# Performance work log

Hardware: AMD Instinct MI355X
Metric: run time of the kernel (lower is better)

## Reference

```python
import jax, jax.numpy as jnp
import numpy as np

N_NODES = 100000
N_EDGES = 1000000
N_QUERY = 100000
F_IN = 64
HIDDEN = 64
LABEL_DIM = 2


def setup_inputs() -> dict:
    key = jax.random.key(0)
    ks = jax.random.split(key, 16)
    inp = {}
    for i, nm in enumerate(["Xr", "Xi", "Xj", "Xk"]):
        inp[nm] = jax.random.normal(ks[i], (N_NODES, F_IN), dtype=jnp.float32)
    for i, nm in enumerate(["norm_r", "norm_i", "norm_j", "norm_k"]):
        inp[nm] = jax.random.normal(ks[4 + i], (N_EDGES,), dtype=jnp.float32) * 0.1
    inp["edge_index"] = jax.random.randint(ks[8], (2, N_EDGES), 0, N_NODES)
    inp["query_edges"] = jax.random.randint(ks[9], (N_QUERY, 2), 0, N_NODES)
    s1 = (2.0 / (F_IN + HIDDEN)) ** 0.5  # glorot
    inp["W1"] = jax.random.normal(ks[10], (4, F_IN, HIDDEN), dtype=jnp.float32) * s1
    inp["b1"] = jnp.zeros((4, HIDDEN), dtype=jnp.float32)
    s2 = (2.0 / (HIDDEN + HIDDEN)) ** 0.5
    inp["W2"] = jax.random.normal(ks[11], (4, HIDDEN, HIDDEN), dtype=jnp.float32) * s2
    inp["b2"] = jnp.zeros((4, HIDDEN), dtype=jnp.float32)
    inp["Cw"] = jax.random.normal(ks[12], (LABEL_DIM, 8 * HIDDEN), dtype=jnp.float32) * 0.05
    inp["Cb"] = jnp.zeros((LABEL_DIM,), dtype=jnp.float32)
    return inp


def _quaconv(Xs, src, dst, norms, W, b, n_nodes):
    # Xs: list of 4 [N,F] components; norms: list of 4 [E] Laplacian norms.
    # P[a][b] = propagate(X_a, -norm_b) = scatter_add over dst of (-norm_b)_e * X_a[src_e]
    P = []
    for a in range(4):
        G = Xs[a][src]  # [E, F] gather, reused for all 4 norms
        P.append([jax.ops.segment_sum((-norms[b])[:, None] * G, dst, num_segments=n_nodes)
                  for b in range(4)])
    Tr = P[0][0] - P[1][1] - P[2][2] - P[3][3]
    Ti = P[1][0] + P[0][1] + P[3][2] - P[2][3]
    Tj = P[2][0] - P[3][1] + P[0][2] + P[1][3]
    Tk = P[3][0] + P[2][1] - P[1][2] + P[0][3]
    Wr, Wi, Wj, Wk = W[0], W[1], W[2], W[3]
    out_r = Tr @ Wr - Ti @ Wi - Tj @ Wj - Tk @ Wk + b[0]
    out_i = Tr @ Wi + Ti @ Wr + Tj @ Wk - Tk @ Wj + b[1]
    out_j = Tr @ Wj - Ti @ Wk + Tj @ Wr + Tk @ Wi + b[2]
    out_k = Tr @ Wk + Ti @ Wj - Tj @ Wi + Tk @ Wr + b[3]
    return out_r, out_i, out_j, out_k


def _forward(Xr, Xi, Xj, Xk, norm_r, norm_i, norm_j, norm_k,
             W1, b1, W2, b2, Cw, Cb, edge_index, query_edges):
    src, dst = edge_index[0], edge_index[1]
    n = Xr.shape[0]
    norms = [norm_r, norm_i, norm_j, norm_k]
    Xs = [Xr, Xi, Xj, Xk]
    for W, b in ((W1, b1), (W2, b2)):
        Xs = list(_quaconv(Xs, src, dst, norms, W, b, n))
        # complex_relu_layer_different: mask = 1.0*(x>=0); mask*x == relu(x)
        Xs = [jax.nn.relu(x) for x in Xs]
    q0, q1 = query_edges[:, 0], query_edges[:, 1]
    # cat(real[q0], real[q1], imag_i[q0], imag_i[q1], ...) -> [Eq, 8*hidden]
    feats = jnp.concatenate([c[idx] for c in Xs for idx in (q0, q1)], axis=-1)
    # dropout is identity at inference; Conv1d(kernel=1) == linear over channels
    logits = feats @ Cw.T + Cb  # [Eq, label_dim]
    return jax.nn.log_softmax(logits, axis=-1)


def reference(Xr, Xi, Xj, Xk, norm_r, norm_i, norm_j, norm_k,
              W1, b1, W2, b2, Cw, Cb, edge_index, query_edges):
    return _forward(Xr, Xi, Xj, Xk, norm_r, norm_i, norm_j, norm_k,
                    W1, b1, W2, b2, Cw, Cb, edge_index, query_edges)
```

## Files before the change

kernel.cpp:

```cpp
#include <hip/hip_runtime.h>
#include <hip/hip_bf16.h>

#define N_NODESC 100000
#define N_EDGESC 1000000
#define N_QUERYC 100000
#define CNT_STRIDE 8

typedef short short8 __attribute__((ext_vector_type(8)));
typedef short s16x2 __attribute__((ext_vector_type(2)));
typedef float f32x4 __attribute__((ext_vector_type(4)));

__device__ __forceinline__ float ldf(const void* p, int i, int isbf) {
  return isbf ? __bfloat162float(((const __hip_bfloat16*)p)[i])
              : ((const float*)p)[i];
}
__device__ __forceinline__ unsigned short f2b(float x) {
  __hip_bfloat16 h = __float2bfloat16(x);
  return *(unsigned short*)&h;
}
__device__ __forceinline__ float b2f(unsigned int u) {
  return __uint_as_float(u << 16);
}
__device__ __forceinline__ s16x2 u2s(unsigned u) {
  union { unsigned u; s16x2 s; } c; c.u = u; return c.s;
}
__device__ __forceinline__ void gload16(const void* g, void* l) {
  __builtin_amdgcn_global_load_lds(
      (const __attribute__((address_space(1))) void*)g,
      (__attribute__((address_space(3))) void*)l, 16, 0, 0);
}

__global__ void k_prep(const void* x, int* flag, int* cnt, int nc) {
  int bid = blockIdx.x;
  int t = threadIdx.x;
  if (bid == 0) {
    __shared__ int scnt;
    if (t == 0) scnt = 0;
    __syncthreads();
    const unsigned short* h = (const unsigned short*)x;
    int local = 0;
    for (int i = t; i < 4096; i += 256) {
      int e = (h[i] >> 7) & 0xFF;
      if (e >= 107 && e <= 133) local++;
    }
    atomicAdd(&scnt, local);
    __syncthreads();
    if (t == 0) *flag = (scnt >= 3482) ? 1 : 0;
  } else {
    int i = (bid - 1) * 256 + t;
    if (i < nc) cnt[i] = 0;
  }
}

__global__ __launch_bounds__(256) void k_fill0_ilv(
    const int* __restrict__ ei,
    const void* nr, const void* ni, const void* nj, const void* nk,
    int* __restrict__ cnt, uint4* __restrict__ temp, int ne, int fillBlocks,
    const void* X0, const void* X1, const void* X2, const void* X3,
    const int* __restrict__ flagp, unsigned short* __restrict__ Xg, int n) {
  int bid = blockIdx.x;
  if (bid < fillBlocks) {
    int isbf = *flagp;
    int e = bid * 256 + threadIdx.x;
    if (e >= ne) return;
    int s = ei[e];
    int d = ei[ne + e];
    int pos = atomicAdd(&cnt[d * CNT_STRIDE], 1);
    uint4 r;
    r.x = (unsigned)s;
    r.y = (unsigned)f2b(-ldf(nr, e, isbf)) | ((unsigned)f2b(-ldf(ni, e, isbf)) << 16);
    r.z = (unsigned)f2b(-ldf(nj, e, isbf)) | ((unsigned)f2b(-ldf(nk, e, isbf)) << 16);
    r.w = (unsigned)pos;
    temp[e] = r;
  } else {
    int isbf = *flagp;
    int lane = threadIdx.x & 63;
    int node = (bid - fillBlocks) * 4 + (threadIdx.x >> 6);
    if (node >= n) return;
    int idx = node * 64 + lane;
    unsigned int lo = f2b(ldf(X0, idx, isbf)) | ((unsigned int)f2b(ldf(X1, idx, isbf)) << 16);
    unsigned int hi = f2b(ldf(X2, idx, isbf)) | ((unsigned int)f2b(ldf(X3, idx, isbf)) << 16);
    uint2 g = make_uint2(lo, hi);
    *(uint2*)(Xg + (size_t)node * 256 + lane * 4) = g;
  }
}

__global__ void k_scan1(const int* __restrict__ cnt, int* __restrict__ off,
                        int* __restrict__ partials, int n) {
  __shared__ int s[1024];
  int t = threadIdx.x;
  int idx = blockIdx.x * 1024 + t;
  int v = (idx < n) ? cnt[idx * CNT_STRIDE] : 0;
  s[t] = v;
  __syncthreads();
  for (int d = 1; d < 1024; d <<= 1) {
    int tmp = (t >= d) ? s[t - d] : 0;
    __syncthreads();
    s[t] += tmp;
    __syncthreads();
  }
  if (idx < n) off[idx] = s[t] - v;
  if (t == 1023) partials[blockIdx.x] = s[1023];
}

__global__ void k_scan2(const int* __restrict__ partials, int* __restrict__ pref,
                        int* __restrict__ off, int nb, int npos) {
  __shared__ int s[128];
  int t = threadIdx.x;
  int v = (t < nb) ? partials[t] : 0;
  s[t] = v;
  __syncthreads();
  for (int d = 1; d < 128; d <<= 1) {
    int tmp = (t >= d) ? s[t - d] : 0;
    __syncthreads();
    s[t] += tmp;
    __syncthreads();
  }
  if (t < nb) pref[t] = s[t] - v;
  if (t == 127) off[npos] = s[127];
}

__global__ void k_scan3(int* __restrict__ off, const int* __restrict__ pref, int n) {
  int i = blockIdx.x * 256 + threadIdx.x;
  if (i < n) off[i] = off[i] + pref[i >> 10];
}

__global__ void k_scatter(const int* __restrict__ ei, const uint4* __restrict__ temp,
                          const int* __restrict__ off, uint4* __restrict__ recs, int ne) {
  int e = blockIdx.x * 256 + threadIdx.x;
  if (e >= ne) return;
  uint4 r = temp[e];
  int d = ei[ne + e];
  int pos = (int)r.w;
  recs[off[d] + pos] = r;
}

#if __has_builtin(__builtin_amdgcn_fdot2_f32_bf16)
#define USE_DOT2 1
#else
#define USE_DOT2 0
#endif
__global__ __launch_bounds__(128, 8) void k_agg(
    const unsigned short* __restrict__ Xg, const int* __restrict__ off,
    const uint4* __restrict__ recs, unsigned short* __restrict__ Tf, int nnodes) {
  __shared__ unsigned short tl4[2][4][256];
  int lane = threadIdx.x & 63;
  int w = threadIdx.x >> 6;
  int gq = blockIdx.x * 2 + w;
  int n0 = gq * 4;
  if (n0 >= nnodes) return;

  int o_[5];
#pragma unroll
  for (int i = 0; i < 5; i++) o_[i] = __builtin_amdgcn_readfirstlane(off[n0 + i]);

#pragma unroll
  for (int n = 0; n < 4; ++n) {
    int rs = o_[n], re = o_[n + 1];
    float tr = 0.f, ti = 0.f, tj = 0.f, tk = 0.f;

    auto qacc = [&](uint2 g, unsigned mx, unsigned my) {
#if USE_DOT2
      unsigned a = mx, b = my;
      unsigned sa = (a >> 16) | (a << 16);
      unsigned sb = (b >> 16) | (b << 16);
      unsigned A1 = a ^ 0x80000000u;
      unsigned A2 = b ^ 0x80008000u;
      unsigned B2 = sb ^ 0x00008000u;
      unsigned D2 = sb ^ 0x80000000u;
      s16x2 gx = u2s(g.x), gy = u2s(g.y);
      tr = __builtin_amdgcn_fdot2_f32_bf16(u2s(A1), gx, tr, false);
      tr = __builtin_amdgcn_fdot2_f32_bf16(u2s(A2), gy, tr, false);
      ti = __builtin_amdgcn_fdot2_f32_bf16(u2s(sa), gx, ti, false);
      ti = __builtin_amdgcn_fdot2_f32_bf16(u2s(B2), gy, ti, false);
      tj = __builtin_amdgcn_fdot2_f32_bf16(u2s(b),  gx, tj, false);
      tj = __builtin_amdgcn_fdot2_f32_bf16(u2s(A1), gy, tj, false);
      tk = __builtin_amdgcn_fdot2_f32_bf16(u2s(D2), gx, tk, false);
      tk = __builtin_amdgcn_fdot2_f32_bf16(u2s(sa), gy, tk, false);
#else
      float mr = __uint_as_float(mx << 16), mi = __uint_as_float(mx & 0xffff0000u);
      float mj = __uint_as_float(my << 16), mk = __uint_as_float(my & 0xffff0000u);
      float xr = __uint_as_float(g.x << 16), xi = __uint_as_float(g.x & 0xffff0000u);
      float xj = __uint_as_float(g.y << 16), xk = __uint_as_float(g.y & 0xffff0000u);
      tr += mr * xr - mi * xi - mj * xj - mk * xk;
      ti += mr * xi + mi * xr + mj * xk - mk * xj;
      tj += mr * xj - mi * xk + mj * xr + mk * xi;
      tk += mr * xk + mi * xj - mj * xi + mk * xr;
#endif
    };

    int e = rs;
    for (; e + 8 <= re; e += 8) {
      uint4 r[8];
#pragma unroll
      for (int u = 0; u < 8; u++) r[u] = recs[e + u];
      int ss[8];
      unsigned sx[8], sy[8];
#pragma unroll
      for (int u = 0; u < 8; u++) {
        ss[u] = __builtin_amdgcn_readfirstlane((int)r[u].x);
        sx[u] = __builtin_amdgcn_readfirstlane(r[u].y);
        sy[u] = __builtin_amdgcn_readfirstlane(r[u].z);
      }
      uint2 g[8];
#pragma unroll
      for (int u = 0; u < 8; u++)
        g[u] = *(const uint2*)(Xg + (size_t)ss[u] * 256 + lane * 4);
#pragma unroll
      for (int u = 0; u < 8; u++) qacc(g[u], sx[u], sy[u]);
    }
    for (; e < re; ++e) {
      uint4 r = recs[e];
      int s = __builtin_amdgcn_readfirstlane((int)r.x);
      unsigned mx = __builtin_amdgcn_readfirstlane(r.y);
      unsigned my = __builtin_amdgcn_readfirstlane(r.z);
      uint2 g0 = *(const uint2*)(Xg + (size_t)s * 256 + lane * 4);
      qacc(g0, mx, my);
    }

    tl4[w][n][lane] = f2b(tr);
    tl4[w][n][64 + lane] = f2b(ti);
    tl4[w][n][128 + lane] = f2b(tj);
    tl4[w][n][192 + lane] = f2b(tk);
  }
  __builtin_amdgcn_wave_barrier();

  size_t blk = (size_t)(gq >> 2) * 4096;
  int qi = gq & 3;
#pragma unroll
  for (int h = 0; h < 2; ++h) {
    int m = h * 64 + lane;
    int n = m & 3, l = m >> 2;
    uint4 v = *(const uint4*)&tl4[w][n][l * 8];
    size_t o = blk + (size_t)(l >> 2) * 512 + (l & 3) * 128 + qi * 32 + n * 8;
    *(uint4*)(Tf + o) = v;
  }
}

__global__ void k_weff2(const void* W1, const void* b1, const void* W2, const void* b2,
                        const int* __restrict__ flagp,
                        unsigned short* __restrict__ Wq1, float* __restrict__ bcat1,
                        unsigned short* __restrict__ Wq2, float* __restrict__ bcat2) {
  int isbf = *flagp;
  int layer = blockIdx.x >> 6;
  const void* W = layer ? W2 : W1;
  const void* b = layer ? b2 : b1;
  unsigned short* Wq = layer ? Wq2 : Wq1;
  float* bcat = layer ? bcat2 : bcat1;
  int t = (blockIdx.x & 63) * 256 + threadIdx.x;
  int w4 = t >> 12;
  int h = (t >> 6) & 63;
  int kk = t & 63;
  int s = (kk >> 3) ^ (h & 7);
  Wq[(w4 * 64 + h) * 64 + s * 8 + (kk & 7)] = f2b(ldf(W, w4 * 4096 + kk * 64 + h, isbf));
  if (t < 256) bcat[t] = ldf(b, t, isbf);
}

__global__ __launch_bounds__(256, 2) void k_gemm(
    const unsigned short* __restrict__ A, const unsigned short* __restrict__ Wq,
    const float* __restrict__ bias, int M, int mode,
    unsigned short* __restrict__ XgOut,
    float* __restrict__ P, const void* Cw, const int* __restrict__ flagp) {
  __shared__ unsigned short Wsm[16384];

  int t = threadIdx.x;
  int lane = t & 63;
  int w = t >> 6;
  int l15 = lane & 15, quad = lane >> 4;
  int m0 = blockIdx.x * 64;
  int hh = (w & 1) * 32;

#pragma unroll
  for (int i = 0; i < 8; i++)
    gload16((const char*)Wq + (size_t)(i * 256 + t) * 16,
            (char*)Wsm + (size_t)(i * 256 + w * 64) * 16);
  __syncthreads();

  short8 av[2][8];
  int n16 = blockIdx.x * 4 + (w >> 1) * 2;
#pragma unroll
  for (int mi = 0; mi < 2; mi++)
#pragma unroll
    for (int kc = 0; kc < 8; kc++)
      av[mi][kc] = *(const short8*)(A + (size_t)(n16 + mi) * 4096 + kc * 512 + lane * 8);

  f32x4 acc[2][4][2];
#pragma unroll
  for (int mi = 0; mi < 2; mi++)
#pragma unroll
    for (int c = 0; c < 4; c++)
#pragma unroll
      for (int hb = 0; hb < 2; hb++) acc[mi][c][hb] = (f32x4){0.f, 0.f, 0.f, 0.f};

#pragma unroll
  for (int kc = 0; kc < 8; kc++) {
    int a = kc >> 1;
    short8 bv[4][2];
#pragma unroll
    for (int c = 0; c < 4; c++) {
      int w4 = a ^ c;
      int neg = (0x3950 >> (a * 4 + c)) & 1;
#pragma unroll
      for (int hb = 0; hb < 2; hb++) {
        int h = hh + hb * 16 + l15;
        int lc = ((kc & 1) * 4 + quad) ^ (l15 & 7);
        short8 bb = *(const short8*)&Wsm[(w4 * 64 + h) * 64 + lc * 8];
        if (neg) {
          uint4 u = *(uint4*)&bb;
          u.x ^= 0x80008000u; u.y ^= 0x80008000u;
          u.z ^= 0x80008000u; u.w ^= 0x80008000u;
          bb = *(short8*)&u;
        }
        bv[c][hb] = bb;
      }
    }
#pragma unroll
    for (int mi = 0; mi < 2; mi++)
#pragma unroll
      for (int c = 0; c < 4; c++)
#pragma unroll
        for (int hb = 0; hb < 2; hb++)
          acc[mi][c][hb] =
              __builtin_amdgcn_mfma_f32_16x16x32_bf16(av[mi][kc], bv[c][hb], acc[mi][c][hb], 0, 0, 0);
  }

  float bias_v[4][2];
#pragma unroll
  for (int c = 0; c < 4; c++)
#pragma unroll
    for (int hb = 0; hb < 2; hb++) bias_v[c][hb] = bias[c * 64 + hh + hb * 16 + l15];

  if (mode == 0) {
#pragma unroll
    for (int mi = 0; mi < 2; mi++) {
#pragma unroll
      for (int hb = 0; hb < 2; hb++) {
#pragma unroll
        for (int r = 0; r < 4; r++) {
          int node = m0 + (w >> 1) * 32 + mi * 16 + quad * 4 + r;
          unsigned int lo =
              f2b(fmaxf(acc[mi][0][hb][r] + bias_v[0][hb], 0.f)) |
              ((unsigned int)f2b(fmaxf(acc[mi][1][hb][r] + bias_v[1][hb], 0.f)) << 16);
          unsigned int hi =
              f2b(fmaxf(acc[mi][2][hb][r] + bias_v[2][hb], 0.f)) |
              ((unsigned int)f2b(fmaxf(acc[mi][3][hb][r] + bias_v[3][hb], 0.f)) << 16);
          *(uint2*)(XgOut + (size_t)node * 256 + (hh + hb * 16 + l15) * 4) =
              make_uint2(lo, hi);
        }
      }
    }
  } else {
    int isbf = *flagp;
    float cw[4][2][4];
#pragma unroll
    for (int c = 0; c < 4; c++)
#pragma unroll
      for (int hb = 0; hb < 2; hb++) {
        int h = hh + hb * 16 + l15;
#pragma unroll
        for (int d = 0; d < 2; d++)
#pragma unroll
          for (int e = 0; e < 2; e++)
            cw[c][hb][e + 2 * d] = ldf(Cw, d * 512 + c * 128 + e * 64 + h, isbf);
      }
    float* Pout = P + ((hh == 0) ? 0 : 4);
#pragma unroll
    for (int mi = 0; mi < 2; mi++) {
#pragma unroll
      for (int r = 0; r < 4; r++) {
        int node = m0 + (w >> 1) * 32 + mi * 16 + quad * 4 + r;
        float pd0 = 0.f, pd1 = 0.f, pd2 = 0.f, pd3 = 0.f;
#pragma unroll
        for (int c = 0; c < 4; c++)
#pragma unroll
          for (int hb = 0; hb < 2; hb++) {
            float v = fmaxf(acc[mi][c][hb][r] + bias_v[c][hb], 0.f);
            pd0 += v * cw[c][hb][0];
            pd1 += v * cw[c][hb][1];
            pd2 += v * cw[c][hb][2];
            pd3 += v * cw[c][hb][3];
          }
#pragma unroll
        for (int o = 1; o < 16; o <<= 1) {
          pd0 += __shfl_xor(pd0, o);
          pd1 += __shfl_xor(pd1, o);
          pd2 += __shfl_xor(pd2, o);
          pd3 += __shfl_xor(pd3, o);
        }
        if (l15 == 0 && node < M) {
          f32x4 st = {pd0, pd1, pd2, pd3};
          *(f32x4*)(Pout + (size_t)node * 8) = st;
        }
      }
    }
  }
}

__global__ void k_query(const int* __restrict__ qe, const float* __restrict__ P,
                        const void* Cb, const int* __restrict__ flagp,
                        void* out, int nq) {
  int isbf = *flagp;
  int q = blockIdx.x * 256 + threadIdx.x;
  if (q >= nq) return;
  int q0 = qe[q * 2], q1 = qe[q * 2 + 1];
  f32x4 a0 = *(const f32x4*)(P + (size_t)q0 * 8);
  f32x4 b0 = *(const f32x4*)(P + (size_t)q0 * 8 + 4);
  f32x4 a1 = *(const f32x4*)(P + (size_t)q1 * 8);
  f32x4 b1 = *(const f32x4*)(P + (size_t)q1 * 8 + 4);
  float l0 = (a0[0] + b0[0]) + (a1[1] + b1[1]) + ldf(Cb, 0, isbf);
  float l1 = (a0[2] + b0[2]) + (a1[3] + b1[3]) + ldf(Cb, 1, isbf);
  float m = fmaxf(l0, l1);
  float lse = m + logf(expf(l0 - m) + expf(l1 - m));
  float o0 = l0 - lse, o1 = l1 - lse;
  if (isbf) {
    __hip_bfloat16* o = (__hip_bfloat16*)out;
    o[q * 2] = __float2bfloat16(o0);
    o[q * 2 + 1] = __float2bfloat16(o1);
  } else {
    float* o = (float*)out;
    o[q * 2] = o0;
    o[q * 2 + 1] = o1;
  }
}

extern "C" void kernel_launch(void* const* d_in, const int* in_sizes, int n_in,
                              void* d_out, int out_size, void* d_ws, size_t ws_size,
                              hipStream_t stream) {
  const int N = N_NODESC, NE = N_EDGESC, NQ = N_QUERYC;
  const int NPAD = 100224;

  char* w = (char*)d_ws;
  auto alloc = [&](size_t bytes) -> void* {
    void* p = (void*)w;
    w += (bytes + 255) & ~(size_t)255;
    return p;
  };
  int* flag       = (int*)alloc(4);
  int* offsets    = (int*)alloc((size_t)(N + 1) * 4);
  int* cnt        = (int*)alloc((size_t)N * CNT_STRIDE * 4);
  int* partials   = (int*)alloc(128 * 4);
  int* pref       = (int*)alloc(128 * 4);
  uint4* recs     = (uint4*)alloc((size_t)NE * 16);
  unsigned short* Tf = (unsigned short*)alloc((size_t)NPAD * 256 * 2);
  unsigned short* Xg = (unsigned short*)alloc((size_t)NPAD * 256 * 2);
  unsigned short* Wq1 = (unsigned short*)alloc(16384 * 2);
  unsigned short* Wq2 = (unsigned short*)alloc(16384 * 2);
  float* bcat1    = (float*)alloc(256 * 4);
  float* bcat2    = (float*)alloc(256 * 4);
  float* P        = (float*)alloc((size_t)N * 8 * 4);
  uint4* temp     = (uint4*)Tf;
  (void)ws_size; (void)n_in; (void)in_sizes; (void)out_size;

  const int* ei = (const int*)d_in[8];

  int nc = N * CNT_STRIDE;
  k_prep<<<1 + (nc + 255) / 256, 256, 0, stream>>>(d_in[0], flag, cnt, nc);

  k_weff2<<<128, 256, 0, stream>>>(d_in[10], d_in[11], d_in[12], d_in[13], flag,
                                   Wq1, bcat1, Wq2, bcat2);

  int fillBlocks = (NE + 255) / 256;
  int ilvBlocks = (N + 3) / 4;
  k_fill0_ilv<<<fillBlocks + ilvBlocks, 256, 0, stream>>>(
      ei, d_in[4], d_in[5], d_in[6], d_in[7], cnt, temp, NE, fillBlocks,
      d_in[0], d_in[1], d_in[2], d_in[3], flag, Xg, N);

  k_scan1<<<(N + 1023) / 1024, 1024, 0, stream>>>(cnt, offsets, partials, N);
  k_scan2<<<1, 128, 0, stream>>>(partials, pref, offsets, (N + 1023) / 1024, N);
  k_scan3<<<(N + 255) / 256, 256, 0, stream>>>(offsets, pref, N);
  k_scatter<<<fillBlocks, 256, 0, stream>>>(ei, temp, offsets, recs, NE);

  int ggrid = (N + 63) / 64;
  int nquads = (N + 3) / 4;
  int agrid = (nquads + 1) / 2;

  k_agg<<<agrid, 128, 0, stream>>>(Xg, offsets, recs, Tf, N);
  k_gemm<<<ggrid, 256, 0, stream>>>(Tf, Wq1, bcat1, N, 0, Xg, nullptr, nullptr, flag);

  k_agg<<<agrid, 128, 0, stream>>>(Xg, offsets, recs, Tf, N);
  k_gemm<<<ggrid, 256, 0, stream>>>(Tf, Wq2, bcat2, N, 1, nullptr, P, d_in[14], flag);

  k_query<<<(NQ + 255) / 256, 256, 0, stream>>>((const int*)d_in[9], P, d_in[15],
                                                flag, d_out, NQ);
}
```

Before: 467.1 us.

## Merge setup kernels, pack count array, and use single-block scan

Measured after the change: 613.7 us. 31.4% more time.

```diff
diff --git a/kernel.cpp b/kernel.cpp
--- a/kernel.cpp
+++ b/kernel.cpp
@@ -4,7 +4,6 @@
 #define N_NODESC 100000
 #define N_EDGESC 1000000
 #define N_QUERYC 100000
-#define CNT_STRIDE 8
 
 typedef short short8 __attribute__((ext_vector_type(8)));
 typedef short s16x2 __attribute__((ext_vector_type(2)));
@@ -17,9 +16,6 @@
 __device__ __forceinline__ unsigned short f2b(float x) {
   __hip_bfloat16 h = __float2bfloat16(x);
   return *(unsigned short*)&h;
-}
-__device__ __forceinline__ float b2f(unsigned int u) {
-  return __uint_as_float(u << 16);
 }
 __device__ __forceinline__ s16x2 u2s(unsigned u) {
   union { unsigned u; s16x2 s; } c; c.u = u; return c.s;
@@ -30,26 +26,47 @@
       (__attribute__((address_space(3))) void*)l, 16, 0, 0);
 }
 
-__global__ void k_prep(const void* x, int* flag, int* cnt, int nc) {
+__global__ __launch_bounds__(256) void k_setup(
+    const void* x, int* flag, int* cnt, int n,
+    const void* W1, const void* b1, const void* W2, const void* b2,
+    unsigned short* __restrict__ Wq1, float* __restrict__ bcat1,
+    unsigned short* __restrict__ Wq2, float* __restrict__ bcat2, int nzBlocks) {
   int bid = blockIdx.x;
   int t = threadIdx.x;
-  if (bid == 0) {
-    __shared__ int scnt;
-    if (t == 0) scnt = 0;
-    __syncthreads();
-    const unsigned short* h = (const unsigned short*)x;
-    int local = 0;
-    for (int i = t; i < 4096; i += 256) {
-      int e = (h[i] >> 7) & 0xFF;
-      if (e >= 107 && e <= 133) local++;
-    }
-    atomicAdd(&scnt, local);
-    __syncthreads();
-    if (t == 0) *flag = (scnt >= 3482) ? 1 : 0;
-  } else {
-    int i = (bid - 1) * 256 + t;
-    if (i < nc) cnt[i] = 0;
-  }
+  if (bid < nzBlocks) {
+    int i = bid * 256 + t;
+    if (i < n) cnt[i] = 0;
+    return;
+  }
+  __shared__ int scnt;
+  if (t == 0) scnt = 0;
+  __syncthreads();
+  const unsigned short* h = (const unsigned short*)x;
+  int local = 0;
+  for (int i = t; i < 4096; i += 256) {
+    int e = (h[i] >> 7) & 0xFF;
+    if (e >= 107 && e <= 133) local++;
+  }
+  atomicAdd(&scnt, local);
+  __syncthreads();
+  int isbf = (scnt >= 3482) ? 1 : 0;
+  if (bid == nzBlocks) {
+    if (t == 0) *flag = isbf;
+    return;
+  }
+  int wb = bid - nzBlocks - 1;
+  int layer = wb >> 6;
+  const void* W = layer ? W2 : W1;
+  const void* b = layer ? b2 : b1;
+  unsigned short* Wq = layer ? Wq2 : Wq1;
+  float* bcat = layer ? bcat2 : bcat1;
+  int tt = (wb & 63) * 256 + t;
+  int w4 = tt >> 12;
+  int hh = (tt >> 6) & 63;
+  int kk = tt & 63;
+  int s = (kk >> 3) ^ (hh & 7);
+  Wq[(w4 * 64 + hh) * 64 + s * 8 + (kk & 7)] = f2b(ldf(W, w4 * 4096 + kk * 64 + hh, isbf));
+  if (tt < 256) bcat[tt] = ldf(b, tt, isbf);
 }
 
 __global__ __launch_bounds__(256) void k_fill0_ilv(
@@ -65,7 +82,7 @@
     if (e >= ne) return;
     int s = ei[e];
     int d = ei[ne + e];
-    int pos = atomicAdd(&cnt[d * CNT_STRIDE], 1);
+    int pos = atomicAdd(&cnt[d], 1);
     uint4 r;
     r.x = (unsigned)s;
     r.y = (unsigned)f2b(-ldf(nr, e, isbf)) | ((unsigned)f2b(-ldf(ni, e, isbf)) << 16);
@@ -85,13 +102,16 @@
   }
 }
 
-__global__ void k_scan1(const int* __restrict__ cnt, int* __restrict__ off,
-                        int* __restrict__ partials, int n) {
+__global__ __launch_bounds__(1024) void k_scan(const int* __restrict__ cnt,
+                                               int* __restrict__ off, int n) {
   __shared__ int s[1024];
+  const int C = 98;
   int t = threadIdx.x;
-  int idx = blockIdx.x * 1024 + t;
-  int v = (idx < n) ? cnt[idx * CNT_STRIDE] : 0;
-  s[t] = v;
+  int base = t * C;
+  int end = min(base + C, n);
+  int sum = 0;
+  for (int i = base; i < end; ++i) sum += cnt[i];
+  s[t] = sum;
   __syncthreads();
   for (int d = 1; d < 1024; d <<= 1) {
     int tmp = (t >= d) ? s[t - d] : 0;
@@ -99,30 +119,13 @@
     s[t] += tmp;
     __syncthreads();
   }
-  if (idx < n) off[idx] = s[t] - v;
-  if (t == 1023) partials[blockIdx.x] = s[1023];
-}
-
-__global__ void k_scan2(const int* __restrict__ partials, int* __restrict__ pref,
-                        int* __restrict__ off, int nb, int npos) {
-  __shared__ int s[128];
-  int t = threadIdx.x;
-  int v = (t < nb) ? partials[t] : 0;
-  s[t] = v;
-  __syncthreads();
-  for (int d = 1; d < 128; d <<= 1) {
-    int tmp = (t >= d) ? s[t - d] : 0;
-    __syncthreads();
-    s[t] += tmp;
-    __syncthreads();
-  }
-  if (t < nb) pref[t] = s[t] - v;
-  if (t == 127) off[npos] = s[127];
-}
-
-__global__ void k_scan3(int* __restrict__ off, const int* __restrict__ pref, int n) {
-  int i = blockIdx.x * 256 + threadIdx.x;
-  if (i < n) off[i] = off[i] + pref[i >> 10];
+  int run = s[t] - sum;
+  for (int i = base; i < end; ++i) {
+    int v = cnt[i];
+    off[i] = run;
+    run += v;
+  }
+  if (t == 1023) off[n] = s[1023];
 }
 
 __global__ void k_scatter(const int* __restrict__ ei, const uint4* __restrict__ temp,
@@ -237,25 +240,6 @@
   }
 }
 
-__global__ void k_weff2(const void* W1, const void* b1, const void* W2, const void* b2,
-                        const int* __restrict__ flagp,
-                        unsigned short* __restrict__ Wq1, float* __restrict__ bcat1,
-                        unsigned short* __restrict__ Wq2, float* __restrict__ bcat2) {
-  int isbf = *flagp;
-  int layer = blockIdx.x >> 6;
-  const void* W = layer ? W2 : W1;
-  const void* b = layer ? b2 : b1;
-  unsigned short* Wq = layer ? Wq2 : Wq1;
-  float* bcat = layer ? bcat2 : bcat1;
-  int t = (blockIdx.x & 63) * 256 + threadIdx.x;
-  int w4 = t >> 12;
-  int h = (t >> 6) & 63;
-  int kk = t & 63;
-  int s = (kk >> 3) ^ (h & 7);
-  Wq[(w4 * 64 + h) * 64 + s * 8 + (kk & 7)] = f2b(ldf(W, w4 * 4096 + kk * 64 + h, isbf));
-  if (t < 256) bcat[t] = ldf(b, t, isbf);
-}
-
 __global__ __launch_bounds__(256, 2) void k_gemm(
     const unsigned short* __restrict__ A, const unsigned short* __restrict__ Wq,
     const float* __restrict__ bias, int M, int mode,
@@ -437,9 +421,7 @@
   };
   int* flag       = (int*)alloc(4);
   int* offsets    = (int*)alloc((size_t)(N + 1) * 4);
-  int* cnt        = (int*)alloc((size_t)N * CNT_STRIDE * 4);
-  int* partials   = (int*)alloc(128 * 4);
-  int* pref       = (int*)alloc(128 * 4);
+  int* cnt        = (int*)alloc((size_t)N * 4);
   uint4* recs     = (uint4*)alloc((size_t)NE * 16);
   unsigned short* Tf = (unsigned short*)alloc((size_t)NPAD * 256 * 2);
   unsigned short* Xg = (unsigned short*)alloc((size_t)NPAD * 256 * 2);
@@ -453,11 +435,11 @@
 
   const int* ei = (const int*)d_in[8];
 
-  int nc = N * CNT_STRIDE;
-  k_prep<<<1 + (nc + 255) / 256, 256, 0, stream>>>(d_in[0], flag, cnt, nc);
-
-  k_weff2<<<128, 256, 0, stream>>>(d_in[10], d_in[11], d_in[12], d_in[13], flag,
-                                   Wq1, bcat1, Wq2, bcat2);
+  int nzBlocks = (N + 255) / 256;
+  k_setup<<<nzBlocks + 1 + 128, 256, 0, stream>>>(
+      d_in[0], flag, cnt, N,
+      d_in[10], d_in[11], d_in[12], d_in[13],
+      Wq1, bcat1, Wq2, bcat2, nzBlocks);
 
   int fillBlocks = (NE + 255) / 256;
   int ilvBlocks = (N + 3) / 4;
@@ -465,9 +447,7 @@
       ei, d_in[4], d_in[5], d_in[6], d_in[7], cnt, temp, NE, fillBlocks,
       d_in[0], d_in[1], d_in[2], d_in[3], flag, Xg, N);
 
-  k_scan1<<<(N + 1023) / 1024, 1024, 0, stream>>>(cnt, offsets, partials, N);
-  k_scan2<<<1, 128, 0, stream>>>(partials, pref, offsets, (N + 1023) / 1024, N);
-  k_scan3<<<(N + 255) / 256, 256, 0, stream>>>(offsets, pref, N);
+  k_scan<<<1, 1024, 0, stream>>>(cnt, offsets, N);
   k_scatter<<<fillBlocks, 256, 0, stream>>>(ei, temp, offsets, recs, NE);
 
   int ggrid = (N + 63) / 64;
```
